# Optimization experiments

Measured on AMD Instinct MI355X. Metric: run time of the kernel, lower is better.

Reference implementation:

```python
import jax, jax.numpy as jnp
import numpy as np

B, L1, L2, H = 32, 512, 512, 768


def setup_inputs() -> dict:
    key = jax.random.key(0)
    k1, k2, k3, k4 = jax.random.split(key, 4)
    x = jax.random.normal(k1, (B, L1, H), dtype=jnp.float32)
    y = jax.random.normal(k2, (B, L2, H), dtype=jnp.float32)
    # y_mask: True = padding position to be masked out (torch masked_fill semantics)
    y_mask = jax.random.randint(k3, (B, L2), 0, 2).astype(bool)
    W = jax.random.normal(k4, (H, H), dtype=jnp.float32) * 0.02  # nn.Linear weight [out,in]
    b = jnp.zeros((H,), dtype=jnp.float32)
    return {"x": x, "y": y, "y_mask": y_mask, "W": W, "b": b}


def reference(x, y, y_mask, W, b):
    # Shared linear projection + ReLU on both sequences (nn.Linear: v @ W^T + b)
    x_proj = jax.nn.relu(jnp.einsum('bmh,oh->bmo', x, W) + b)
    y_proj = jax.nn.relu(jnp.einsum('bnh,oh->bno', y, W) + b)
    # Unscaled attention scores [B, L1, L2]
    scores = jnp.einsum('bmh,bnh->bmn', x_proj, y_proj)
    scores = jnp.where(y_mask[:, None, :], -jnp.inf, scores)
    alpha = jax.nn.softmax(scores, axis=-1)
    # Attention-weighted sum over the *original* y (not y_proj)
    matched_seq = jnp.einsum('bmn,bnh->bmh', alpha, y)
    return matched_seq
```

## Files before the change

kernel.cpp:

```cpp
#include <hip/hip_runtime.h>
#include <hip/hip_bf16.h>
#include <math.h>


typedef _Float16 f16x8 __attribute__((ext_vector_type(8)));
typedef float f32x4 __attribute__((ext_vector_type(4)));

__device__ __forceinline__ void gld_lds16(const void* g, void* l) {
  __builtin_amdgcn_global_load_lds(
      (const __attribute__((address_space(1))) unsigned*)g,
      (__attribute__((address_space(3))) unsigned*)l, 16, 0, 0);
}

__global__ __launch_bounds__(256) void cvt_xy_kernel(
    const float* __restrict__ x, const float* __restrict__ y,
    _Float16* __restrict__ xh, _Float16* __restrict__ yh) {
  const float* src = blockIdx.y ? y : x;
  _Float16* dst = blockIdx.y ? yh : xh;
  size_t i = ((size_t)blockIdx.x * 256 + threadIdx.x) * 8;
  float4 a = *(const float4*)&src[i];
  float4 b = *(const float4*)&src[i + 4];
  _Float16 h[8] = {(_Float16)a.x, (_Float16)a.y, (_Float16)a.z, (_Float16)a.w,
                   (_Float16)b.x, (_Float16)b.y, (_Float16)b.z, (_Float16)b.w};
  *(uint4*)&dst[i] = *(uint4*)h;
}

__global__ __launch_bounds__(256) void cvt_f16_kernel(
    const float* __restrict__ src, _Float16* __restrict__ dst) {
  size_t i = ((size_t)blockIdx.x * 256 + threadIdx.x) * 8;
  float4 a = *(const float4*)&src[i];
  float4 b = *(const float4*)&src[i + 4];
  _Float16 h[8] = {(_Float16)a.x, (_Float16)a.y, (_Float16)a.z, (_Float16)a.w,
                   (_Float16)b.x, (_Float16)b.y, (_Float16)b.z, (_Float16)b.w};
  *(uint4*)&dst[i] = *(uint4*)h;
}

__global__ __launch_bounds__(256) void proj_mfma_kernel(
    const _Float16* __restrict__ Xh, const _Float16* __restrict__ Yh,
    const _Float16* __restrict__ W, const float* __restrict__ bias,
    _Float16* __restrict__ Px, _Float16* __restrict__ Py) {
  const int K = 768, N = 768;
  const _Float16* A = blockIdx.z ? Yh : Xh;
  _Float16* P = blockIdx.z ? Py : Px;
  __shared__ _Float16 As[128 * 32], Bs[128 * 32];
  int bm = blockIdx.x * 128, bn = blockIdx.y * 128;
  int tid = threadIdx.x, lane = tid & 63, wave = tid >> 6;
  int wm = (wave & 1) * 64, wn = (wave >> 1) * 64;
  int fr = lane & 15, fk = (lane >> 4) * 8;
  int lrow = lane >> 2, lcol = (lane & 3) << 3;

  f32x4 acc[4][4];
#pragma unroll
  for (int i = 0; i < 4; ++i)
#pragma unroll
    for (int j = 0; j < 4; ++j)
#pragma unroll
      for (int e = 0; e < 4; ++e) acc[i][j][e] = 0.f;

  for (int k0 = 0; k0 < K; k0 += 32) {
    __syncthreads();
#pragma unroll
    for (int t = 0; t < 2; ++t) {
      int row = wave * 32 + t * 16;
      gld_lds16(&A[(size_t)(bm + row + lrow) * K + k0 + lcol], &As[row * 32]);
      gld_lds16(&W[(size_t)(bn + row + lrow) * K + k0 + lcol], &Bs[row * 32]);
    }
    __syncthreads();
    f16x8 a[4], bb[4];
#pragma unroll
    for (int i = 0; i < 4; ++i) {
      a[i] = *(const f16x8*)&As[(wm + i * 16 + fr) * 32 + fk];
      bb[i] = *(const f16x8*)&Bs[(wn + i * 16 + fr) * 32 + fk];
    }
#pragma unroll
    for (int i = 0; i < 4; ++i)
#pragma unroll
      for (int j = 0; j < 4; ++j)
        acc[i][j] = __builtin_amdgcn_mfma_f32_16x16x32_f16(a[i], bb[j], acc[i][j], 0, 0, 0);
  }
#pragma unroll
  for (int i = 0; i < 4; ++i)
#pragma unroll
    for (int r = 0; r < 4; ++r) {
      int m = bm + wm + i * 16 + (lane >> 4) * 4 + r;
#pragma unroll
      for (int j = 0; j < 4; ++j) {
        int n = bn + wn + j * 16 + fr;
        P[(size_t)m * N + n] = (_Float16)fmaxf(acc[i][j][r] + bias[n], 0.f);
      }
    }
}

__global__ __launch_bounds__(512) void scores_softmax_kernel(
    const _Float16* __restrict__ Px, const _Float16* __restrict__ Py,
    const int* __restrict__ mask, _Float16* __restrict__ Alpha) {
  const int K = 768, L = 512;
  __shared__ _Float16 As[64 * 32];
  __shared__ _Float16 Bs[512 * 32];
  __shared__ float redm[8][64], reds[8][64];
  int b = blockIdx.y;
  size_t pb = (size_t)b * L * K;
  const int* mk = mask + (size_t)b * L;
  _Float16* Ab = Alpha + (size_t)b * L * L;
  int bm = blockIdx.x * 64;
  int tid = threadIdx.x, lane = tid & 63, wave = tid >> 6;
  int wn = wave * 64;
  int fr = lane & 15, fk = (lane >> 4) * 8;
  int lrow = lane >> 2, lcol = (lane & 3) << 3;

  f32x4 acc[4][4];
#pragma unroll
  for (int i = 0; i < 4; ++i)
#pragma unroll
    for (int j = 0; j < 4; ++j)
#pragma unroll
      for (int e = 0; e < 4; ++e) acc[i][j][e] = 0.f;

  for (int k0 = 0; k0 < K; k0 += 32) {
    __syncthreads();
#pragma unroll
    for (int t = 0; t < 4; ++t) {
      int row = wave * 64 + t * 16;
      gld_lds16(&Py[pb + (size_t)(row + lrow) * K + k0 + lcol], &Bs[row * 32]);
    }
    if (wave < 4) {
      int row = wave * 16;
      gld_lds16(&Px[pb + (size_t)(bm + row + lrow) * K + k0 + lcol], &As[row * 32]);
    }
    __syncthreads();
    f16x8 a[4], bb[4];
#pragma unroll
    for (int i = 0; i < 4; ++i) {
      a[i] = *(const f16x8*)&As[(i * 16 + fr) * 32 + fk];
      bb[i] = *(const f16x8*)&Bs[(wn + i * 16 + fr) * 32 + fk];
    }
#pragma unroll
    for (int i = 0; i < 4; ++i)
#pragma unroll
      for (int j = 0; j < 4; ++j)
        acc[i][j] = __builtin_amdgcn_mfma_f32_16x16x32_f16(a[i], bb[j], acc[i][j], 0, 0, 0);
  }

  int mki[4];
#pragma unroll
  for (int j = 0; j < 4; ++j) mki[j] = mk[wn + j * 16 + fr];
#pragma unroll
  for (int i = 0; i < 4; ++i)
#pragma unroll
    for (int j = 0; j < 4; ++j)
      if (mki[j]) {
#pragma unroll
        for (int r = 0; r < 4; ++r) acc[i][j][r] = -INFINITY;
      }

  int g4 = (lane >> 4) << 2;
#pragma unroll
  for (int i = 0; i < 4; ++i)
#pragma unroll
    for (int r = 0; r < 4; ++r) {
      float m = fmaxf(fmaxf(acc[i][0][r], acc[i][1][r]),
                      fmaxf(acc[i][2][r], acc[i][3][r]));
      m = fmaxf(m, __shfl_xor(m, 1));
      m = fmaxf(m, __shfl_xor(m, 2));
      m = fmaxf(m, __shfl_xor(m, 4));
      m = fmaxf(m, __shfl_xor(m, 8));
      if (fr == 0) redm[wave][i * 16 + g4 + r] = m;
    }
  __syncthreads();
  float M[4][4];
#pragma unroll
  for (int i = 0; i < 4; ++i)
#pragma unroll
    for (int r = 0; r < 4; ++r) {
      int row = i * 16 + g4 + r;
      float m = redm[0][row];
#pragma unroll
      for (int w = 1; w < 8; ++w) m = fmaxf(m, redm[w][row]);
      M[i][r] = m;
    }
#pragma unroll
  for (int i = 0; i < 4; ++i)
#pragma unroll
    for (int r = 0; r < 4; ++r) {
      float s = 0.f;
#pragma unroll
      for (int j = 0; j < 4; ++j) {
        float e = __expf(acc[i][j][r] - M[i][r]);
        acc[i][j][r] = e;
        s += e;
      }
      s += __shfl_xor(s, 1);
      s += __shfl_xor(s, 2);
      s += __shfl_xor(s, 4);
      s += __shfl_xor(s, 8);
      if (fr == 0) reds[wave][i * 16 + g4 + r] = s;
    }
  __syncthreads();
#pragma unroll
  for (int i = 0; i < 4; ++i)
#pragma unroll
    for (int r = 0; r < 4; ++r) {
      int row = i * 16 + g4 + r;
      float s = reds[0][row];
#pragma unroll
      for (int w = 1; w < 8; ++w) s += reds[w][row];
      float inv = 1.0f / s;
#pragma unroll
      for (int j = 0; j < 4; ++j)
        Ab[(size_t)(bm + row) * L + wn + j * 16 + fr] =
            (_Float16)(acc[i][j][r] * inv);
    }
}

__global__ __launch_bounds__(256) void yT_kernel(
    const _Float16* __restrict__ Yh, _Float16* __restrict__ YT) {
  __shared__ unsigned short T[64][65];
  int b = blockIdx.z;
  int n0 = blockIdx.x * 64, h0 = blockIdx.y * 64;
  const unsigned short* Yb = (const unsigned short*)Yh + (size_t)b * 512 * 768;
  unsigned short* Tb = (unsigned short*)YT + (size_t)b * 768 * 512;
  int tid = threadIdx.x;
  int r = tid >> 4, c = (tid & 15) << 2;
#pragma unroll
  for (int i = 0; i < 4; ++i) {
    int rr = r + i * 16;
    ushort4 v = *(const ushort4*)&Yb[(size_t)(n0 + rr) * 768 + h0 + c];
    T[c + 0][rr] = v.x;
    T[c + 1][rr] = v.y;
    T[c + 2][rr] = v.z;
    T[c + 3][rr] = v.w;
  }
  __syncthreads();
  int hr = tid >> 2, nc = (tid & 3) << 4;
  unsigned short tmp[16];
#pragma unroll
  for (int j = 0; j < 16; ++j) tmp[j] = T[hr][nc + j];
  unsigned short* dst = &Tb[(size_t)(h0 + hr) * 512 + n0 + nc];
  *(uint4*)&dst[0] = *(uint4*)&tmp[0];
  *(uint4*)&dst[8] = *(uint4*)&tmp[8];
}

__global__ __launch_bounds__(256) void attn_mfma_kernel(
    const _Float16* __restrict__ Alpha, const _Float16* __restrict__ YT,
    float* __restrict__ O) {
  const int L = 512, H = 768;
  __shared__ _Float16 As[128 * 32], Bs[128 * 32];
  int b = blockIdx.z;
  const _Float16* Ab = Alpha + (size_t)b * L * L;
  const _Float16* Yb = YT + (size_t)b * H * L;
  float* Ob = O + (size_t)b * L * H;
  int bm = blockIdx.x * 128, bn = blockIdx.y * 128;
  int tid = threadIdx.x, lane = tid & 63, wave = tid >> 6;
  int wm = (wave & 1) * 64, wn = (wave >> 1) * 64;
  int fr = lane & 15, fk = (lane >> 4) * 8;
  int lrow = lane >> 2, lcol = (lane & 3) << 3;

  f32x4 acc[4][4];
#pragma unroll
  for (int i = 0; i < 4; ++i)
#pragma unroll
    for (int j = 0; j < 4; ++j)
#pragma unroll
      for (int e = 0; e < 4; ++e) acc[i][j][e] = 0.f;

  for (int k0 = 0; k0 < L; k0 += 32) {
    __syncthreads();
#pragma unroll
    for (int t = 0; t < 2; ++t) {
      int row = wave * 32 + t * 16;
      gld_lds16(&Ab[(size_t)(bm + row + lrow) * L + k0 + lcol], &As[row * 32]);
      gld_lds16(&Yb[(size_t)(bn + row + lrow) * L + k0 + lcol], &Bs[row * 32]);
    }
    __syncthreads();
    f16x8 a[4], bb[4];
#pragma unroll
    for (int i = 0; i < 4; ++i) {
      a[i] = *(const f16x8*)&As[(wm + i * 16 + fr) * 32 + fk];
      bb[i] = *(const f16x8*)&Bs[(wn + i * 16 + fr) * 32 + fk];
    }
#pragma unroll
    for (int i = 0; i < 4; ++i)
#pragma unroll
      for (int j = 0; j < 4; ++j)
        acc[i][j] = __builtin_amdgcn_mfma_f32_16x16x32_f16(a[i], bb[j], acc[i][j], 0, 0, 0);
  }
#pragma unroll
  for (int i = 0; i < 4; ++i)
#pragma unroll
    for (int r = 0; r < 4; ++r) {
      int m = bm + wm + i * 16 + (lane >> 4) * 4 + r;
#pragma unroll
      for (int j = 0; j < 4; ++j) {
        int h = bn + wn + j * 16 + fr;
        Ob[(size_t)m * H + h] = acc[i][j][r];
      }
    }
}

extern "C" void kernel_launch(void* const* d_in, const int* in_sizes, int n_in,
                              void* d_out, int out_size, void* d_ws, size_t ws_size,
                              hipStream_t stream) {
  const float* x = (const float*)d_in[0];
  const float* y = (const float*)d_in[1];
  const int* y_mask = (const int*)d_in[2];
  const float* W = (const float*)d_in[3];
  const float* b = (const float*)d_in[4];
  float* out = (float*)d_out;

  const size_t E = (size_t)16384 * 768;
  _Float16* xh = (_Float16*)d_ws;
  _Float16* yh = xh + E;
  _Float16* Px = yh + E;
  _Float16* Py = Px + E;
  _Float16* Wh = Py + E;
  _Float16* alpha = xh;
  _Float16* yT = Px;

  dim3 blk(256);
  cvt_xy_kernel<<<dim3(6144, 2), blk, 0, stream>>>(x, y, xh, yh);
  cvt_f16_kernel<<<dim3(288), blk, 0, stream>>>(W, Wh);
  proj_mfma_kernel<<<dim3(128, 6, 2), blk, 0, stream>>>(xh, yh, Wh, b, Px, Py);
  scores_softmax_kernel<<<dim3(8, 32), dim3(512), 0, stream>>>(Px, Py, y_mask, alpha);
  yT_kernel<<<dim3(8, 12, 32), blk, 0, stream>>>(yh, yT);
  attn_mfma_kernel<<<dim3(4, 6, 32), blk, 0, stream>>>(alpha, yT, out);
}
```

Baseline: 288.6 us.

## Rewrite projection GEMM as 256x256 double-buffered 8-wave pipelined kernel

Replaces the 128x128, single-buffered projection GEMM with a 256x256 tile, 512-thread kernel. It uses 128 KB of dynamic LDS with double buffering, XOR-swizzled LDS layout and interleaved global-to-LDS prefetch between quarter MFMA phases. It also adds explicit waitcnt and sched barriers plus setprio around the MFMA bursts. The aim is to hide load latency, raise arithmetic intensity and avoid LDS bank conflicts. In exchange, occupancy drops and fewer blocks are launched (384), and the hand-written synchronization is fragile.

```diff
diff --git a/kernel.cpp b/kernel.cpp
--- a/kernel.cpp
+++ b/kernel.cpp
@@ -11,6 +11,22 @@
       (const __attribute__((address_space(1))) unsigned*)g,
       (__attribute__((address_space(3))) unsigned*)l, 16, 0, 0);
 }
+
+#define BARR()                          \
+  do {                                  \
+    __builtin_amdgcn_s_barrier();       \
+    __builtin_amdgcn_sched_barrier(0);  \
+  } while (0)
+#define LGKM0()                                      \
+  do {                                               \
+    asm volatile("s_waitcnt lgkmcnt(0)" ::: "memory"); \
+    __builtin_amdgcn_sched_barrier(0);               \
+  } while (0)
+#define VMW(n)                                            \
+  do {                                                    \
+    asm volatile("s_waitcnt vmcnt(" #n ")" ::: "memory"); \
+    __builtin_amdgcn_sched_barrier(0);                    \
+  } while (0)
 
 __global__ __launch_bounds__(256) void cvt_xy_kernel(
     const float* __restrict__ x, const float* __restrict__ y,
@@ -35,58 +51,151 @@
   *(uint4*)&dst[i] = *(uint4*)h;
 }
 
-__global__ __launch_bounds__(256) void proj_mfma_kernel(
+
+__device__ __forceinline__ void stage_half(const _Float16* __restrict__ G,
+                                           int grow0, int k0, _Float16* L,
+                                           int w, int l) {
+#pragma unroll
+  for (int s = 0; s < 2; ++s) {
+    int rb = s * 64 + w * 8;
+    int rin = rb + (l >> 3);
+    int cp = (l & 7) ^ ((rin >> 1) & 6);
+    gld_lds16(&G[(size_t)(grow0 + rin) * 768 + k0 + cp * 8],
+              L + (size_t)rb * 64);
+  }
+}
+
+__device__ __forceinline__ f16x8 frag_ld(const _Float16* S, int row, int colb) {
+  int off = row * 128 + colb;
+  off ^= (off >> 4) & 0x60;
+  return *(const f16x8*)((const char*)S + off);
+}
+
+__device__ __forceinline__ void read_a(const _Float16* S, int wm, int mh,
+                                       int fr, int fkg, f16x8 a[4][2]) {
+#pragma unroll
+  for (int f4 = 0; f4 < 4; ++f4)
+#pragma unroll
+    for (int ks = 0; ks < 2; ++ks)
+      a[f4][ks] = frag_ld(S, wm + mh * 64 + f4 * 16 + fr, ks * 64 + fkg * 16);
+}
+
+__device__ __forceinline__ void read_b(const _Float16* S, int wn, int nh,
+                                       int fr, int fkg, f16x8 b[2][2]) {
+#pragma unroll
+  for (int nb = 0; nb < 2; ++nb)
+#pragma unroll
+    for (int ks = 0; ks < 2; ++ks)
+      b[nb][ks] = frag_ld(S, wn + (nh * 2 + nb) * 16 + fr, ks * 64 + fkg * 16);
+}
+
+__device__ __forceinline__ void mma_q(f16x8 a[4][2], f16x8 b[2][2],
+                                      f32x4 acc[8][4], int mh, int nh) {
+  __builtin_amdgcn_s_setprio(1);
+#pragma unroll
+  for (int f4 = 0; f4 < 4; ++f4)
+#pragma unroll
+    for (int nb = 0; nb < 2; ++nb)
+#pragma unroll
+      for (int ks = 0; ks < 2; ++ks)
+        acc[mh * 4 + f4][nh * 2 + nb] = __builtin_amdgcn_mfma_f32_16x16x32_f16(
+            a[f4][ks], b[nb][ks], acc[mh * 4 + f4][nh * 2 + nb], 0, 0, 0);
+  __builtin_amdgcn_s_setprio(0);
+}
+
+__global__ __launch_bounds__(512, 2) void proj8_kernel(
     const _Float16* __restrict__ Xh, const _Float16* __restrict__ Yh,
     const _Float16* __restrict__ W, const float* __restrict__ bias,
     _Float16* __restrict__ Px, _Float16* __restrict__ Py) {
-  const int K = 768, N = 768;
+  const int N = 768;
   const _Float16* A = blockIdx.z ? Yh : Xh;
   _Float16* P = blockIdx.z ? Py : Px;
-  __shared__ _Float16 As[128 * 32], Bs[128 * 32];
-  int bm = blockIdx.x * 128, bn = blockIdx.y * 128;
-  int tid = threadIdx.x, lane = tid & 63, wave = tid >> 6;
-  int wm = (wave & 1) * 64, wn = (wave >> 1) * 64;
-  int fr = lane & 15, fk = (lane >> 4) * 8;
-  int lrow = lane >> 2, lcol = (lane & 3) << 3;
-
-  f32x4 acc[4][4];
-#pragma unroll
-  for (int i = 0; i < 4; ++i)
+  extern __shared__ _Float16 smem[];
+  _Float16* As0 = smem;
+  _Float16* As1 = smem + 16384;
+  _Float16* Bs0 = smem + 32768;
+  _Float16* Bs1 = smem + 49152;
+
+  const int bm = blockIdx.x * 256, bn = blockIdx.y * 256;
+  const int tid = threadIdx.x, l = tid & 63, w = tid >> 6;
+  const int fr = l & 15, fkg = l >> 4;
+  const int wm = (w >> 2) * 128, wn = (w & 3) * 64;
+
+  f32x4 acc[8][4];
+#pragma unroll
+  for (int i = 0; i < 8; ++i)
 #pragma unroll
     for (int j = 0; j < 4; ++j)
 #pragma unroll
       for (int e = 0; e < 4; ++e) acc[i][j][e] = 0.f;
 
-  for (int k0 = 0; k0 < K; k0 += 32) {
-    __syncthreads();
-#pragma unroll
-    for (int t = 0; t < 2; ++t) {
-      int row = wave * 32 + t * 16;
-      gld_lds16(&A[(size_t)(bm + row + lrow) * K + k0 + lcol], &As[row * 32]);
-      gld_lds16(&W[(size_t)(bn + row + lrow) * K + k0 + lcol], &Bs[row * 32]);
-    }
-    __syncthreads();
-    f16x8 a[4], bb[4];
-#pragma unroll
-    for (int i = 0; i < 4; ++i) {
-      a[i] = *(const f16x8*)&As[(wm + i * 16 + fr) * 32 + fk];
-      bb[i] = *(const f16x8*)&Bs[(wn + i * 16 + fr) * 32 + fk];
-    }
-#pragma unroll
-    for (int i = 0; i < 4; ++i)
-#pragma unroll
-      for (int j = 0; j < 4; ++j)
-        acc[i][j] = __builtin_amdgcn_mfma_f32_16x16x32_f16(a[i], bb[j], acc[i][j], 0, 0, 0);
-  }
-#pragma unroll
-  for (int i = 0; i < 4; ++i)
-#pragma unroll
-    for (int r = 0; r < 4; ++r) {
-      int m = bm + wm + i * 16 + (lane >> 4) * 4 + r;
-#pragma unroll
-      for (int j = 0; j < 4; ++j) {
-        int n = bn + wn + j * 16 + fr;
-        P[(size_t)m * N + n] = (_Float16)fmaxf(acc[i][j][r] + bias[n], 0.f);
+  stage_half(A, bm + 0, 0, As0, w, l);
+  stage_half(A, bm + 128, 0, As0 + 128 * 64, w, l);
+  stage_half(W, bn + 0, 0, Bs0, w, l);
+  stage_half(W, bn + 128, 0, Bs0 + 128 * 64, w, l);
+  stage_half(W, bn + 0, 64, Bs1, w, l);
+  stage_half(W, bn + 128, 64, Bs1 + 128 * 64, w, l);
+  VMW(4);
+  BARR();
+
+  f16x8 a[4][2], b0[2][2], b1[2][2];
+
+  for (int t = 0; t < 6; ++t) {
+    const bool g = (t < 5);
+    const int ka1 = (2 * t + 1) * 64, k2 = (2 * t + 2) * 64, k3 = (2 * t + 3) * 64;
+    read_a(As0, wm, 0, fr, fkg, a);
+    read_b(Bs0, wn, 0, fr, fkg, b0);
+    stage_half(A, bm + 0, ka1, As1, w, l);
+    BARR(); LGKM0();
+    mma_q(a, b0, acc, 0, 0);
+    BARR();
+    read_b(Bs0, wn, 1, fr, fkg, b1);
+    stage_half(A, bm + 128, ka1, As1 + 128 * 64, w, l);
+    BARR(); LGKM0();
+    mma_q(a, b1, acc, 0, 1);
+    BARR();
+    read_a(As0, wm, 1, fr, fkg, a);
+    if (g) stage_half(W, bn + 0, k2, Bs0, w, l);
+    BARR(); LGKM0();
+    mma_q(a, b1, acc, 1, 1);
+    BARR();
+    if (g) stage_half(W, bn + 128, k2, Bs0 + 128 * 64, w, l);
+    BARR(); LGKM0();
+    mma_q(a, b0, acc, 1, 0);
+    if (g) { VMW(4); } else { VMW(0); }
+    BARR();
+    read_a(As1, wm, 0, fr, fkg, a);
+    read_b(Bs1, wn, 0, fr, fkg, b0);
+    if (g) stage_half(A, bm + 0, k2, As0, w, l);
+    BARR(); LGKM0();
+    mma_q(a, b0, acc, 0, 0);
+    BARR();
+    read_b(Bs1, wn, 1, fr, fkg, b1);
+    if (g) stage_half(A, bm + 128, k2, As0 + 128 * 64, w, l);
+    BARR(); LGKM0();
+    mma_q(a, b1, acc, 0, 1);
+    BARR();
+    read_a(As1, wm, 1, fr, fkg, a);
+    if (g) stage_half(W, bn + 0, k3, Bs1, w, l);
+    BARR(); LGKM0();
+    mma_q(a, b1, acc, 1, 1);
+    BARR();
+    if (g) stage_half(W, bn + 128, k3, Bs1 + 128 * 64, w, l);
+    BARR(); LGKM0();
+    mma_q(a, b0, acc, 1, 0);
+    if (g) VMW(4);
+    BARR();
+  }
+
+#pragma unroll
+  for (int mf = 0; mf < 8; ++mf)
+#pragma unroll
+    for (int r = 0; r < 4; ++r) {
+      int m = bm + wm + mf * 16 + fkg * 4 + r;
+#pragma unroll
+      for (int nf = 0; nf < 4; ++nf) {
+        int n = bn + wn + nf * 16 + fr;
+        P[(size_t)m * N + n] = (_Float16)fmaxf(acc[mf][nf][r] + bias[n], 0.f);
       }
     }
 }
@@ -175,7 +284,7 @@
       int row = i * 16 + g4 + r;
       float m = redm[0][row];
 #pragma unroll
-      for (int w = 1; w < 8; ++w) m = fmaxf(m, redm[w][row]);
+      for (int ww = 1; ww < 8; ++ww) m = fmaxf(m, redm[ww][row]);
       M[i][r] = m;
     }
 #pragma unroll
@@ -203,7 +312,7 @@
       int row = i * 16 + g4 + r;
       float s = reds[0][row];
 #pragma unroll
-      for (int w = 1; w < 8; ++w) s += reds[w][row];
+      for (int ww = 1; ww < 8; ++ww) s += reds[ww][row];
       float inv = 1.0f / s;
 #pragma unroll
       for (int j = 0; j < 4; ++j)
@@ -316,10 +425,17 @@
   _Float16* alpha = xh;
   _Float16* yT = Px;
 
+  static bool attr_set = false;
+  if (!attr_set) {
+    hipFuncSetAttribute((const void*)proj8_kernel,
+                        hipFuncAttributeMaxDynamicSharedMemorySize, 131072);
+    attr_set = true;
+  }
+
   dim3 blk(256);
   cvt_xy_kernel<<<dim3(6144, 2), blk, 0, stream>>>(x, y, xh, yh);
   cvt_f16_kernel<<<dim3(288), blk, 0, stream>>>(W, Wh);
-  proj_mfma_kernel<<<dim3(128, 6, 2), blk, 0, stream>>>(xh, yh, Wh, b, Px, Py);
+  proj8_kernel<<<dim3(64, 3, 2), dim3(512), 131072, stream>>>(xh, yh, Wh, b, Px, Py);
   scores_softmax_kernel<<<dim3(8, 32), dim3(512), 0, stream>>>(Px, Py, y_mask, alpha);
   yT_kernel<<<dim3(8, 12, 32), blk, 0, stream>>>(yh, yT);
   attn_mfma_kernel<<<dim3(4, 6, 32), blk, 0, stream>>>(alpha, yT, out);
```

Result: slower. 337.3 us (+16.9%).
